# Kernel tuning notes

Hardware: AMD Instinct MI355X
Metric: run time of the kernel (lower is better)

The kernel has to match this reference:

```python
import jax, jax.numpy as jnp
import numpy as np

V, D, T, B, MS, WIN, EOS = 10000, 256, 128, 8, 4, 1, 4
S = MS + 1          # decoder segment length (y_input0 + MAX_SEGMENT tokens)
HRATE = 0.1
LOGINF = 1e6


def setup_inputs() -> dict:
    key = jax.random.key(0)
    ks = jax.random.split(key, 17)
    s = lambda i, shape: (jax.random.normal(ks[i], shape, jnp.float32) * 0.05)
    return dict(
        x_ids=jax.random.randint(ks[0], (B, T + 2 * WIN), 0, V),
        lens=jnp.full((B,), T, dtype=jnp.int32),
        emb=s(1, (V, D)),
        y_start=s(2, (1, D)),
        cell_Wi=s(3, (4 * D, D)), cell_Wh=s(4, (4 * D, D)), cell_b=s(5, (4 * D,)),
        yin0_W=s(6, (D, D)), yin0_b=s(7, (D,)),
        hlin_W=s(8, (2 * D, D)), hlin_b=s(9, (2 * D,)),
        l0_Wi=s(10, (4 * D, D)), l0_Wh=s(11, (4 * D, D)), l0_b=s(12, (4 * D,)),
        l1_Wi=s(13, (4 * D, D)), l1_Wh=s(14, (4 * D, D)), l1_b=s(15, (4 * D,)),
        out_b=s(16, (V,)),
    )


def _cell(x, h, c, Wi, Wh, b):
    # torch LSTM gate order: i, f, g, o
    g = x @ Wi.T + h @ Wh.T + b
    i, f, gg, o = jnp.split(g, 4, axis=-1)
    c2 = jax.nn.sigmoid(f) * c + jax.nn.sigmoid(i) * jnp.tanh(gg)
    return jax.nn.sigmoid(o) * jnp.tanh(c2), c2


def reference(x_ids, lens, emb, y_start, cell_Wi, cell_Wh, cell_b,
              yin0_W, yin0_b, hlin_W, hlin_b,
              l0_Wi, l0_Wh, l0_b, l1_Wi, l1_Wh, l1_b, out_b):
    y = x_ids[:, WIN:-WIN]                     # [B, T] target ids
    x = emb[y]                                 # [B, T, D]

    # --- encoder LSTMCell scan over j_start (state persists across schedule) ---
    seq = jnp.concatenate(
        [jnp.broadcast_to(y_start, (B, D))[None], jnp.transpose(x, (1, 0, 2))[:-1]], 0)  # [T,B,D]
    z = jnp.zeros((B, D), x.dtype)
    def enc_step(carry, xt):
        h, c = carry
        h2, c2 = _cell(xt, h, c, cell_Wi, cell_Wh, cell_b)
        return (h2, c2), h2
    _, h_seq = jax.lax.scan(enc_step, (z, z), seq)        # [T, B, D]

    drop_h = HRATE * h_seq
    y_in0 = drop_h @ yin0_W.T + yin0_b                    # [T, B, D]
    h0_all = jnp.tanh(drop_h @ hlin_W.T + hlin_b).reshape(T, B, 2, D)  # per-layer init h

    # --- build decoder inputs [T, B, S, D]: (y_input0, x[j_start:j_start+MS]) ---
    xp = jnp.pad(x, ((0, 0), (0, MS), (0, 0)))            # zero-pad time (causal => pads don't affect valid outputs)
    pos = jnp.arange(T)[:, None] + jnp.arange(MS)[None, :]           # [T, MS]
    seg_x = jnp.transpose(xp[:, pos], (1, 0, 2, 3))       # [T, B, MS, D]
    seg = jnp.concatenate([y_in0[:, :, None, :], seg_x], axis=2)     # [T, B, S, D]

    # --- 2-layer LSTM decoder, vmapped over j_start ---
    def decode(seg_t, h_init):                            # seg_t [B,S,D], h_init [B,2,D]
        def step(carry, xt):
            (h0, c0), (h1, c1) = carry
            h0n, c0n = _cell(xt, h0, c0, l0_Wi, l0_Wh, l0_b)
            h1n, c1n = _cell(h0n, h1, c1, l1_Wi, l1_Wh, l1_b)
            return ((h0n, c0n), (h1n, c1n)), h1n
        init = ((h_init[:, 0], z), (h_init[:, 1], z))
        _, hs = jax.lax.scan(step, init, jnp.transpose(seg_t, (1, 0, 2)))
        return jnp.transpose(hs, (1, 0, 2))               # [B, S, D]
    dec_h = jax.vmap(decode)(seg, h0_all)                 # [T, B, S, D]

    # --- tied output projection + log-softmax (only needed gathers kept) ---
    logits = jnp.einsum('tbsd,vd->tbsv', dec_h, emb) + out_b         # [T,B,S,V]
    logZ = jax.nn.logsumexp(logits, axis=-1)                          # [T,B,S]

    tgt = jnp.transpose(y[:, jnp.clip(pos, 0, T - 1)], (1, 0, 2))     # [T,B,MS]
    tgt_lp = jnp.take_along_axis(logits[:, :, :MS, :], tgt[..., None], axis=3)[..., 0] \
             - logZ[:, :, :MS]                                        # [T,B,MS]
    pmask = (pos < T)[:, None, :]
    cum = jnp.cumsum(jnp.where(pmask, tgt_lp, 0.0), axis=2)           # [T,B,MS]
    eos_lp = logits[:, :, 1:, EOS] - logZ[:, :, 1:]                   # [T,B,MS]

    kmask = (jnp.arange(T)[:, None] + jnp.arange(1, MS + 1)[None, :]) <= T   # [T,MS]
    body = jnp.where(kmask[:, None, :], cum + eos_lp, -LOGINF)        # [T,B,MS]
    logpy = jnp.concatenate([jnp.full((T, 1, B), -LOGINF, body.dtype),
                             jnp.transpose(body, (0, 2, 1))], axis=1)  # [T, MS+1, B]

    # --- alpha forward DP: alpha[j] = logsumexp_L alpha[j-L] + logpy[j-L][L] ---
    jj = jnp.arange(1, T + 1)[:, None]
    ii = jnp.arange(MS)[None, :]
    sstart = jj - MS + ii                                             # [T,MS]
    LPG = jnp.where((sstart >= 0)[..., None],
                    logpy[jnp.clip(sstart, 0), jnp.broadcast_to(MS - ii, (T, MS))],
                    -LOGINF)                                          # [T,MS,B]

    Apad0 = jnp.full((MS + T + 1, B), -LOGINF, logpy.dtype).at[MS].set(0.0)
    def dp_step(Apad, args):
        j, lpg = args
        win = jax.lax.dynamic_slice(Apad, (j, 0), (MS, B))            # alpha[j-MS .. j-1]
        aj = jax.nn.logsumexp(win + lpg, axis=0)
        return jax.lax.dynamic_update_slice(Apad, aj[None], (MS + j, 0)), None
    Apad, _ = jax.lax.scan(dp_step, Apad0, (jnp.arange(1, T + 1), LPG))
    alpha = Apad[MS:]                                                 # [T+1, B]

    ret = -jnp.sum(alpha[lens, jnp.arange(B)]) / jnp.sum(lens).astype(alpha.dtype)
    return ret
```

## Files before the change

kernel.cpp:

```cpp
#include <hip/hip_runtime.h>

#define V_ 10000
#define D_ 256
#define T_ 128
#define B_ 8
#define MS_ 4
#define S_ 5
#define EOS_ 4

typedef unsigned short b16_t;
typedef __attribute__((ext_vector_type(8))) short s16x8;
typedef __attribute__((ext_vector_type(8))) unsigned short u16x8;
typedef __attribute__((ext_vector_type(4))) float f32x4;
typedef __attribute__((ext_vector_type(2))) _Float16 h16x2;

__device__ inline b16_t f2bf(float f) {
  union { float f; unsigned u; } v; v.f = f;
  unsigned r = v.u + 0x7FFFu + ((v.u >> 16) & 1u);
  return (b16_t)(r >> 16);
}
__device__ inline float bf2f(b16_t h) {
  union { unsigned u; float f; } v; v.u = ((unsigned)h) << 16; return v.f;
}
__device__ inline float sigm_(float x) { return 1.0f / (1.0f + __expf(-x)); }
__device__ inline float tanh_(float x) { return 2.0f / (1.0f + __expf(-2.0f * x)) - 1.0f; }
__device__ inline h16x2 bch(unsigned u) { return __builtin_bit_cast(h16x2, u); }
__device__ inline unsigned pkh(float a, float b) {
  h16x2 v; v.x = (_Float16)a; v.y = (_Float16)b;
  return __builtin_bit_cast(unsigned, v);
}

#if __has_builtin(__builtin_amdgcn_fdot2)
#define FDOT2(a, b, c) __builtin_amdgcn_fdot2((a), (b), (c), false)
#else
#define FDOT2(a, b, c) ((c) + (float)(a).x * (float)(b).x + (float)(a).y * (float)(b).y)
#endif

__device__ inline float qswap1(float x) {
  return __builtin_bit_cast(float, __builtin_amdgcn_update_dpp(
      0, __builtin_bit_cast(int, x), 0xB1, 0xF, 0xF, true));
}

__device__ inline void cvt4(const float* __restrict__ s, b16_t* __restrict__ d) {
  float4 v = *(const float4*)s;
  ushort4 o = { f2bf(v.x), f2bf(v.y), f2bf(v.z), f2bf(v.w) };
  *(ushort4*)d = o;
}

__global__ void k_prep(const float* __restrict__ emb, const float* __restrict__ cWi,
                       const float* __restrict__ y0W, const float* __restrict__ hlW,
                       const float* __restrict__ l0Wi, const float* __restrict__ l0Wh,
                       const float* __restrict__ l1Wi, const float* __restrict__ l1Wh,
                       const float* __restrict__ cWh, const int* __restrict__ x_ids,
                       const float* __restrict__ y_st,
                       b16_t* __restrict__ emb_bf, b16_t* __restrict__ cWi_bf,
                       b16_t* __restrict__ y0W_bf, b16_t* __restrict__ hlW_bf,
                       b16_t* __restrict__ l0Wi_bf, b16_t* __restrict__ l0Wh_bf,
                       b16_t* __restrict__ Wcat_bf, unsigned* __restrict__ Whf,
                       b16_t* __restrict__ seq_bf, b16_t* __restrict__ seg_bf) {
  for (long i = (long)blockIdx.x * blockDim.x + threadIdx.x; i < 1410048L;
       i += (long)gridDim.x * blockDim.x) {
    if (i < 640000L) { cvt4(emb + i * 4, emb_bf + i * 4); }
    else if (i < 705536L) { long j = i - 640000L; cvt4(cWi + j * 4, cWi_bf + j * 4); }
    else if (i < 721920L) { long j = i - 705536L; cvt4(y0W + j * 4, y0W_bf + j * 4); }
    else if (i < 754688L) { long j = i - 721920L; cvt4(hlW + j * 4, hlW_bf + j * 4); }
    else if (i < 820224L) { long j = i - 754688L; cvt4(l0Wi + j * 4, l0Wi_bf + j * 4); }
    else if (i < 885760L) { long j = i - 820224L; cvt4(l0Wh + j * 4, l0Wh_bf + j * 4); }
    else if (i < 1016832L) {
      long j = (i - 885760L) * 4;
      long n = j >> 9; int k = (int)(j & 511);
      const float* src = (k < 256) ? (l1Wi + n * 256 + k) : (l1Wh + n * 256 + (k - 256));
      cvt4(src, Wcat_bf + j);
    } else if (i < 1082368L) {
      long j = i - 1016832L;
      float4 v = *(const float4*)(cWh + j * 4);
      Whf[2 * j] = pkh(v.x, v.y);
      Whf[2 * j + 1] = pkh(v.z, v.w);
    } else if (i < 1147904L) {
      long j = i - 1082368L;
      int m = (int)(j >> 6), c = (int)(j & 63) * 4;
      int t = m >> 3, b = m & 7;
      const float* src = (t == 0) ? (y_st + c)
                                  : (emb + (size_t)x_ids[b * (T_ + 2) + t] * D_ + c);
      cvt4(src, seq_bf + (size_t)m * D_ + c);
    } else {
      long j = i - 1147904L;
      int r = (int)(j >> 6), c = (int)(j & 63) * 4;
      int p = r >> 2, s = 1 + (r & 3);
      int t = p >> 3, b = p & 7;
      int tt = t + s - 1;
      int ps = r + (r >> 2) + 1;
      if (tt < T_) {
        int tok = x_ids[b * (T_ + 2) + tt + 1];
        cvt4(emb + (size_t)tok * D_ + c, seg_bf + (size_t)ps * 256 + c);
      } else {
        ushort4 z = {0, 0, 0, 0};
        *(ushort4*)(seg_bf + (size_t)ps * 256 + c) = z;
      }
    }
  }
}

__global__ __launch_bounds__(256) void k_gemm(const b16_t* __restrict__ A, int lda,
                                              const b16_t* __restrict__ Bw,
                                              const float* __restrict__ bias,
                                              float* __restrict__ C, int ldc) {
  __shared__ b16_t As[64][264];
  __shared__ b16_t Bs[64][264];
  int tid = threadIdx.x;
  int rowBase = blockIdx.x * 64, colBase = blockIdx.y * 64;
  for (int i = tid; i < 64 * 32; i += 256) {
    int r = i >> 5, c = (i & 31) * 8;
    *(u16x8*)&As[r][c] = *(const u16x8*)(A + (size_t)(rowBase + r) * lda + c);
    *(u16x8*)&Bs[r][c] = *(const u16x8*)(Bw + (size_t)(colBase + r) * 256 + c);
  }
  __syncthreads();
  int w = tid >> 6, l = tid & 63, lr = l & 15, kg = l >> 4;
  f32x4 acc[4] = {{0.f,0.f,0.f,0.f},{0.f,0.f,0.f,0.f},{0.f,0.f,0.f,0.f},{0.f,0.f,0.f,0.f}};
  for (int kk = 0; kk < 8; ++kk) {
    s16x8 a = *(const s16x8*)&As[w * 16 + lr][kk * 32 + kg * 8];
#pragma unroll
    for (int f = 0; f < 4; ++f) {
      s16x8 b = *(const s16x8*)&Bs[f * 16 + lr][kk * 32 + kg * 8];
      acc[f] = __builtin_amdgcn_mfma_f32_16x16x32_bf16(a, b, acc[f], 0, 0, 0);
    }
  }
#pragma unroll
  for (int f = 0; f < 4; ++f) {
#pragma unroll
    for (int r = 0; r < 4; ++r) {
      int m = rowBase + w * 16 + kg * 4 + r;
      int n = colBase + f * 16 + lr;
      C[(size_t)m * ldc + n] = acc[f][r] + bias[n];
    }
  }
}

#define ENC_CH4(i0)                                                            \
  do {                                                                         \
    uint4 a0 = hp[i0], a1 = hp[i0 + 1], a2 = hp[i0 + 2], a3 = hp[i0 + 3];      \
    s0 = FDOT2(bch(a0.x), bch(wv[4 * (i0) + 0]), s0);                          \
    s1 = FDOT2(bch(a0.y), bch(wv[4 * (i0) + 1]), s1);                          \
    s0 = FDOT2(bch(a0.z), bch(wv[4 * (i0) + 2]), s0);                          \
    s1 = FDOT2(bch(a0.w), bch(wv[4 * (i0) + 3]), s1);                          \
    s0 = FDOT2(bch(a1.x), bch(wv[4 * (i0) + 4]), s0);                          \
    s1 = FDOT2(bch(a1.y), bch(wv[4 * (i0) + 5]), s1);                          \
    s0 = FDOT2(bch(a1.z), bch(wv[4 * (i0) + 6]), s0);                          \
    s1 = FDOT2(bch(a1.w), bch(wv[4 * (i0) + 7]), s1);                          \
    s0 = FDOT2(bch(a2.x), bch(wv[4 * (i0) + 8]), s0);                          \
    s1 = FDOT2(bch(a2.y), bch(wv[4 * (i0) + 9]), s1);                          \
    s0 = FDOT2(bch(a2.z), bch(wv[4 * (i0) + 10]), s0);                         \
    s1 = FDOT2(bch(a2.w), bch(wv[4 * (i0) + 11]), s1);                         \
    s0 = FDOT2(bch(a3.x), bch(wv[4 * (i0) + 12]), s0);                         \
    s1 = FDOT2(bch(a3.y), bch(wv[4 * (i0) + 13]), s1);                         \
    s0 = FDOT2(bch(a3.z), bch(wv[4 * (i0) + 14]), s0);                         \
    s1 = FDOT2(bch(a3.w), bch(wv[4 * (i0) + 15]), s1);                         \
  } while (0)

struct EncS { unsigned hbuf[128]; float gl[256]; };
struct GemS { b16_t As[64][264]; b16_t Bs[64][264]; };

__global__ __launch_bounds__(512, 2) void k_enc_x0(
    const unsigned* __restrict__ Whf,
    const float* __restrict__ encX,
    unsigned* __restrict__ hglob,
    b16_t* __restrict__ droph,
    const b16_t* __restrict__ seg_bf, const b16_t* __restrict__ l0Wi_bf,
    const float* __restrict__ l0b, float* __restrict__ X0) {
  __shared__ union { EncS e; GemS g; } sm;
  int tid = threadIdx.x;
  if (blockIdx.x < 32) {
    int b = blockIdx.x & 7, q = blockIdx.x >> 3;
    int r = tid >> 1, ch = tid & 1;
    int growr = ((r >> 6) << 8) + q * 64 + (r & 63);
    unsigned wv[64];
    {
      const uint4* wp = (const uint4*)(Whf + (size_t)growr * 128 + ch * 64);
#pragma unroll
      for (int i = 0; i < 16; ++i) {
        uint4 v = wp[i];
        wv[4*i] = v.x; wv[4*i+1] = v.y; wv[4*i+2] = v.z; wv[4*i+3] = v.w;
      }
    }
#pragma unroll
    for (int i = 0; i < 64; ++i) asm volatile("" : "+v"(wv[i]));
    if (tid < 128) sm.e.hbuf[tid] = 0;
    float c = 0.f;
    float ex = encX[(size_t)b * 1024 + growr];
    __syncthreads();
#pragma unroll 1
    for (int t = 0; t < 128; ++t) {
      const uint4* hp = (const uint4*)&sm.e.hbuf[ch * 64];
      float s0 = 0.f, s1 = 0.f;
      ENC_CH4(0);
      __builtin_amdgcn_sched_barrier(0);
      ENC_CH4(4);
      __builtin_amdgcn_sched_barrier(0);
      ENC_CH4(8);
      __builtin_amdgcn_sched_barrier(0);
      ENC_CH4(12);
      float sum = s0 + s1;
      sum += qswap1(sum);
      if (ch == 0) sm.e.gl[r] = sum + ex;
      __syncthreads();
      if (tid < 64) {
        float gi = sm.e.gl[tid], gf = sm.e.gl[64 + tid];
        float gg = sm.e.gl[128 + tid], go = sm.e.gl[192 + tid];
        float c2 = sigm_(gf) * c + sigm_(gi) * tanh_(gg);
        float h2 = sigm_(go) * tanh_(c2);
        c = c2;
        float hnb = qswap1(h2);
        if ((tid & 1) == 0) {
          unsigned pk = pkh(h2, hnb) | 0x00010001u;
          sm.e.hbuf[q * 32 + (tid >> 1)] = pk;
          if (t < 127)
            __hip_atomic_store(&hglob[(((size_t)t * 8 + b) * 4 + q) * 32 + (tid >> 1)],
                               pk, __ATOMIC_RELAXED, __HIP_MEMORY_SCOPE_AGENT);
        }
        droph[((size_t)t * 8 + b) * 256 + q * 64 + tid] = f2bf(0.1f * h2);
      }
      if (t < 127) {
        if (tid >= 64 && tid < 160) {
          int idx = tid - 64;
          int ro = idx >> 5;
          int rq = ro + (ro >= q);
          int dw = idx & 31;
          unsigned* src = &hglob[(((size_t)t * 8 + b) * 4 + rq) * 32 + dw];
          unsigned v;
          do {
            v = __hip_atomic_load(src, __ATOMIC_RELAXED, __HIP_MEMORY_SCOPE_AGENT);
          } while (v == 0u);
          sm.e.hbuf[rq * 32 + dw] = v;
        }
        ex = encX[((size_t)(t + 1) * 8 + b) * 1024 + growr];
        __syncthreads();
      }
    }
  } else {
    int bx2 = blockIdx.x - 32;
    int rb = (bx2 & 63) * 64;
    int colBase = (bx2 >> 6) * 64;
    if (tid < 256) {
      for (int i = tid; i < 64 * 32; i += 256) {
        int r = i >> 5, cc = (i & 31) * 8;
        int jj = rb + r, ps = jj + (jj >> 2) + 1;
        *(u16x8*)&sm.g.As[r][cc] = *(const u16x8*)(seg_bf + (size_t)ps * 256 + cc);
        *(u16x8*)&sm.g.Bs[r][cc] = *(const u16x8*)(l0Wi_bf + (size_t)(colBase + r) * 256 + cc);
      }
    }
    __syncthreads();
    if (tid < 256) {
      int w = tid >> 6, l = tid & 63, lr = l & 15, kg = l >> 4;
      f32x4 acc[4] = {{0.f,0.f,0.f,0.f},{0.f,0.f,0.f,0.f},{0.f,0.f,0.f,0.f},{0.f,0.f,0.f,0.f}};
      for (int kk = 0; kk < 8; ++kk) {
        s16x8 a = *(const s16x8*)&sm.g.As[w * 16 + lr][kk * 32 + kg * 8];
#pragma unroll
        for (int f = 0; f < 4; ++f) {
          s16x8 b = *(const s16x8*)&sm.g.Bs[f * 16 + lr][kk * 32 + kg * 8];
          acc[f] = __builtin_amdgcn_mfma_f32_16x16x32_bf16(a, b, acc[f], 0, 0, 0);
        }
      }
#pragma unroll
      for (int f = 0; f < 4; ++f) {
#pragma unroll
        for (int r = 0; r < 4; ++r) {
          int jj = rb + w * 16 + kg * 4 + r;
          int ps = jj + (jj >> 2) + 1;
          int n = colBase + f * 16 + lr;
          X0[(size_t)ps * 1024 + n] = acc[f][r] + l0b[n];
        }
      }
    }
  }
}

__global__ __launch_bounds__(256) void k_proj(
    const b16_t* __restrict__ droph, const b16_t* __restrict__ y0W_bf,
    const float* __restrict__ y0b, const b16_t* __restrict__ hlW_bf,
    const float* __restrict__ hlb, b16_t* __restrict__ seg_bf,
    b16_t* __restrict__ hcat,
    const b16_t* __restrict__ l0Wi_bf, const float* __restrict__ l0b,
    float* __restrict__ X0) {
  __shared__ b16_t As[64][264];
  __shared__ b16_t Bs[64][264];
  int bx = blockIdx.x, by = blockIdx.y;
  const b16_t* Ab; int lda;
  const b16_t* Bw; const float* bias; int colBase, mode;
  if (by < 4)       { Ab = droph;  lda = 256;  Bw = y0W_bf;  bias = y0b; colBase = by * 64;        mode = 0; }
  else if (by < 12) { Ab = droph;  lda = 256;  Bw = hlW_bf;  bias = hlb; colBase = (by - 4) * 64;  mode = 1; }
  else              { Ab = seg_bf; lda = 1280; Bw = l0Wi_bf; bias = l0b; colBase = (by - 12) * 64; mode = 2; }
  int rowBase = bx * 64;
  int tid = threadIdx.x;
  for (int i = tid; i < 64 * 32; i += 256) {
    int r = i >> 5, c = (i & 31) * 8;
    *(u16x8*)&As[r][c] = *(const u16x8*)(Ab + (size_t)(rowBase + r) * lda + c);
    *(u16x8*)&Bs[r][c] = *(const u16x8*)(Bw + (size_t)(colBase + r) * 256 + c);
  }
  __syncthreads();
  int w = tid >> 6, l = tid & 63, lr = l & 15, kg = l >> 4;
  f32x4 acc[4] = {{0.f,0.f,0.f,0.f},{0.f,0.f,0.f,0.f},{0.f,0.f,0.f,0.f},{0.f,0.f,0.f,0.f}};
  for (int kk = 0; kk < 8; ++kk) {
    s16x8 a = *(const s16x8*)&As[w * 16 + lr][kk * 32 + kg * 8];
#pragma unroll
    for (int f = 0; f < 4; ++f) {
      s16x8 b = *(const s16x8*)&Bs[f * 16 + lr][kk * 32 + kg * 8];
      acc[f] = __builtin_amdgcn_mfma_f32_16x16x32_bf16(a, b, acc[f], 0, 0, 0);
    }
  }
#pragma unroll
  for (int f = 0; f < 4; ++f) {
#pragma unroll
    for (int r = 0; r < 4; ++r) {
      int m = rowBase + w * 16 + kg * 4 + r;
      int n = colBase + f * 16 + lr;
      float v = acc[f][r] + bias[n];
      if (mode == 0) seg_bf[(size_t)m * 1280 + n] = f2bf(v);
      else if (mode == 1) hcat[(size_t)m * 512 + n] = f2bf(tanh_(v));
      else X0[(size_t)m * 5120 + n] = v;
    }
  }
}

__global__ __launch_bounds__(512) void k_dec2(
    b16_t* __restrict__ hcat,
    const b16_t* __restrict__ l0Wh_bf,
    const b16_t* __restrict__ Wcat_bf,
    const float* __restrict__ X0,
    const float* __restrict__ l1b,
    float* __restrict__ c0, float* __restrict__ c1,
    b16_t* __restrict__ dec_out, int s) {
  __shared__ b16_t A0s[16][264];
  __shared__ b16_t A1s[16][520];
  int tid = threadIdx.x;
  int R0 = blockIdx.x * 16;
  for (int i = tid; i < 16 * 32; i += 512) {
    int r = i >> 5, cc = (i & 31) * 8;
    *(u16x8*)&A0s[r][cc] = *(const u16x8*)(hcat + (size_t)(R0 + r) * 512 + cc);
    *(u16x8*)&A1s[r][256 + cc] = *(const u16x8*)(hcat + (size_t)(R0 + r) * 512 + 256 + cc);
  }
  __syncthreads();
  int w = tid >> 6, l = tid & 63, lr = l & 15, kg = l >> 4;
  {
    s16x8 af[8];
#pragma unroll
    for (int kk = 0; kk < 8; ++kk)
      af[kk] = *(const s16x8*)&A0s[lr][kk * 32 + kg * 8];
    f32x4 acc[4][2];
#pragma unroll
    for (int g = 0; g < 4; ++g)
#pragma unroll
      for (int ct = 0; ct < 2; ++ct) acc[g][ct] = f32x4{0.f, 0.f, 0.f, 0.f};
#pragma unroll
    for (int g = 0; g < 4; ++g)
#pragma unroll
      for (int ct = 0; ct < 2; ++ct) {
        int n = g * 256 + w * 32 + ct * 16 + lr;
        const b16_t* bp = l0Wh_bf + (size_t)n * 256 + kg * 8;
#pragma unroll
        for (int kk = 0; kk < 8; ++kk)
          acc[g][ct] = __builtin_amdgcn_mfma_f32_16x16x32_bf16(
              af[kk], *(const s16x8*)(bp + kk * 32), acc[g][ct], 0, 0, 0);
      }
#pragma unroll
    for (int ct = 0; ct < 2; ++ct)
#pragma unroll
      for (int r = 0; r < 4; ++r) {
        int row = kg * 4 + r, p = R0 + row, d = w * 32 + ct * 16 + lr;
        const float* xp = X0 + ((size_t)p * 5 + s) * 1024;
        float gi = acc[0][ct][r] + xp[d],       gf = acc[1][ct][r] + xp[256 + d];
        float gg = acc[2][ct][r] + xp[512 + d], go = acc[3][ct][r] + xp[768 + d];
        float cc0 = c0[(size_t)p * 256 + d];
        float c2 = sigm_(gf) * cc0 + sigm_(gi) * tanh_(gg);
        float h2 = sigm_(go) * tanh_(c2);
        c0[(size_t)p * 256 + d] = c2;
        b16_t hb = f2bf(h2);
        A1s[row][d] = hb;
        hcat[(size_t)p * 512 + d] = hb;
      }
  }
  __syncthreads();
  {
    s16x8 a1[16];
#pragma unroll
    for (int kk = 0; kk < 16; ++kk)
      a1[kk] = *(const s16x8*)&A1s[lr][kk * 32 + kg * 8];
    f32x4 acc[4][2];
#pragma unroll
    for (int g = 0; g < 4; ++g)
#pragma unroll
      for (int ct = 0; ct < 2; ++ct) acc[g][ct] = f32x4{0.f, 0.f, 0.f, 0.f};
#pragma unroll
    for (int g = 0; g < 4; ++g)
#pragma unroll
      for (int ct = 0; ct < 2; ++ct) {
        int n = g * 256 + w * 32 + ct * 16 + lr;
        const b16_t* bp = Wcat_bf + (size_t)n * 512 + kg * 8;
#pragma unroll
        for (int kk = 0; kk < 16; ++kk)
          acc[g][ct] = __builtin_amdgcn_mfma_f32_16x16x32_bf16(
              a1[kk], *(const s16x8*)(bp + kk * 32), acc[g][ct], 0, 0, 0);
      }
#pragma unroll
    for (int ct = 0; ct < 2; ++ct)
#pragma unroll
      for (int r = 0; r < 4; ++r) {
        int row = kg * 4 + r, p = R0 + row, d = w * 32 + ct * 16 + lr;
        float gi = acc[0][ct][r] + l1b[d],       gf = acc[1][ct][r] + l1b[256 + d];
        float gg = acc[2][ct][r] + l1b[512 + d], go = acc[3][ct][r] + l1b[768 + d];
        float cc1 = c1[(size_t)p * 256 + d];
        float c2 = sigm_(gf) * cc1 + sigm_(gi) * tanh_(gg);
        float h2 = sigm_(go) * tanh_(c2);
        c1[(size_t)p * 256 + d] = c2;
        b16_t hb = f2bf(h2);
        hcat[(size_t)p * 512 + 256 + d] = hb;
        dec_out[((size_t)p * 5 + s) * 256 + d] = hb;
      }
  }
}

__global__ __launch_bounds__(512) void k_logits_ext(
    const b16_t* __restrict__ Abf, const b16_t* __restrict__ emb_bf,
    const float* __restrict__ out_b, float* __restrict__ sumexp,
    const int* __restrict__ x_ids, float* __restrict__ tl,
    float* __restrict__ el) {
  int bid = blockIdx.x;
  int tid = threadIdx.x;
  if (bid < 560) {
    __shared__ b16_t Bs[64][264];
    int rowBase = (bid % 40) * 128;
    int w = tid >> 6, l = tid & 63, lr = l & 15, kg = l >> 4;
    s16x8 af[8];
    {
      const b16_t* arow = Abf + (size_t)(rowBase + w * 16 + lr) * 256;
#pragma unroll
      for (int kk = 0; kk < 8; ++kk) af[kk] = *(const s16x8*)(arow + kk * 32 + kg * 8);
    }
    float runsum[4] = {0.f, 0.f, 0.f, 0.f};
    int t0 = (bid / 40) * 12, t1 = (t0 + 12 < 157) ? (t0 + 12) : 157;
    for (int tile = t0; tile < t1; ++tile) {
      int colBase = tile * 64;
      __syncthreads();
      for (int i = tid; i < 64 * 32; i += 512) {
        int r = i >> 5, cc = (i & 31) * 8;
        int vrow = colBase + r;
        u16x8 bv = {0, 0, 0, 0, 0, 0, 0, 0};
        if (vrow < V_) bv = *(const u16x8*)(emb_bf + (size_t)vrow * D_ + cc);
        *(u16x8*)&Bs[r][cc] = bv;
      }
      __syncthreads();
      f32x4 acc[4] = {{0.f,0.f,0.f,0.f},{0.f,0.f,0.f,0.f},{0.f,0.f,0.f,0.f},{0.f,0.f,0.f,0.f}};
#pragma unroll
      for (int kk = 0; kk < 8; ++kk) {
#pragma unroll
        for (int f = 0; f < 4; ++f) {
          s16x8 b = *(const s16x8*)&Bs[f * 16 + lr][kk * 32 + kg * 8];
          acc[f] = __builtin_amdgcn_mfma_f32_16x16x32_bf16(af[kk], b, acc[f], 0, 0, 0);
        }
      }
#pragma unroll
      for (int f = 0; f < 4; ++f) {
        int n = colBase + f * 16 + lr;
        if (n < V_) {
          float ob = out_b[n];
#pragma unroll
          for (int r = 0; r < 4; ++r) runsum[r] += __expf(acc[f][r] + ob);
        }
      }
    }
#pragma unroll
    for (int r = 0; r < 4; ++r) {
      float rs = runsum[r];
      rs += __shfl_xor(rs, 1, 64);
      rs += __shfl_xor(rs, 2, 64);
      rs += __shfl_xor(rs, 4, 64);
      rs += __shfl_xor(rs, 8, 64);
      if (lr == 0) atomicAdd(&sumexp[rowBase + w * 16 + kg * 4 + r], rs);
    }
  } else {
    int p = (bid - 560) * 8 + (tid >> 6);
    int lane = tid & 63;
    int t = p >> 3, b = p & 7;
    for (int s = 0; s < S_; ++s) {
      const b16_t* hr = Abf + ((size_t)p * S_ + s) * D_;
      float hv[4];
#pragma unroll
      for (int j = 0; j < 4; ++j) hv[j] = bf2f(hr[lane * 4 + j]);
      if (s < MS_) {
        int pos = t + s; if (pos > T_ - 1) pos = T_ - 1;
        int tok = x_ids[b * (T_ + 2) + pos + 1];
        const b16_t* er = emb_bf + (size_t)tok * D_;
        float ps = 0.f;
#pragma unroll
        for (int j = 0; j < 4; ++j) ps += hv[j] * bf2f(er[lane * 4 + j]);
        for (int m = 1; m < 64; m <<= 1) ps += __shfl_xor(ps, m, 64);
        if (lane == 0) tl[p * MS_ + s] = ps + out_b[tok];
      }
      if (s >= 1) {
        const b16_t* er = emb_bf + (size_t)EOS_ * D_;
        float ps = 0.f;
#pragma unroll
        for (int j = 0; j < 4; ++j) ps += hv[j] * bf2f(er[lane * 4 + j]);
        for (int m = 1; m < 64; m <<= 1) ps += __shfl_xor(ps, m, 64);
        if (lane == 0) el[p * MS_ + (s - 1)] = ps + out_b[EOS_];
      }
    }
  }
}

__global__ __launch_bounds__(256) void k_final(const float* __restrict__ sumexp,
                                               const float* __restrict__ tl,
                                               const float* __restrict__ el,
                                               const int* __restrict__ lens,
                                               float* __restrict__ out) {
  __shared__ float logpy[T_][S_][B_];
  __shared__ float alpha[T_ + 1][B_];
  int tid = threadIdx.x;
  for (int p = tid; p < T_ * B_; p += 256) {
    int t = p >> 3, b = p & 7;
    float lz[S_];
#pragma unroll
    for (int s = 0; s < S_; ++s) lz[s] = __logf(sumexp[p * S_ + s]);
    float cum = 0.f, cums[MS_];
#pragma unroll
    for (int s = 0; s < MS_; ++s) {
      float tlp = tl[p * MS_ + s] - lz[s];
      if (t + s < T_) cum += tlp;
      cums[s] = cum;
    }
#pragma unroll
    for (int k = 1; k <= MS_; ++k) {
      float bv = -1000000.0f;
      if (t + k <= T_) bv = cums[k - 1] + (el[p * MS_ + (k - 1)] - lz[k]);
      logpy[t][k][b] = bv;
    }
  }
  __syncthreads();
  if (tid < B_) {
    int b = tid;
    alpha[0][b] = 0.f;
    for (int j = 1; j <= T_; ++j) {
      float vs[MS_], vmax = -1e30f;
#pragma unroll
      for (int k = 1; k <= MS_; ++k) {
        float vv = -2000000.0f;
        if (j - k >= 0) vv = alpha[j - k][b] + logpy[j - k][k][b];
        vs[k - 1] = vv;
        if (vv > vmax) vmax = vv;
      }
      float ssum = 0.f;
#pragma unroll
      for (int k = 0; k < MS_; ++k) ssum += __expf(vs[k] - vmax);
      alpha[j][b] = vmax + __logf(ssum);
    }
  }
  __syncthreads();
  if (tid == 0) {
    float num = 0.f, den = 0.f;
    for (int b = 0; b < B_; ++b) { num += alpha[lens[b]][b]; den += (float)lens[b]; }
    out[0] = -num / den;
  }
}

extern "C" void kernel_launch(void* const* d_in, const int* in_sizes, int n_in,
                              void* d_out, int out_size, void* d_ws, size_t ws_size,
                              hipStream_t stream) {
  const int* x_ids   = (const int*)d_in[0];
  const int* lens    = (const int*)d_in[1];
  const float* emb   = (const float*)d_in[2];
  const float* y_st  = (const float*)d_in[3];
  const float* cWi   = (const float*)d_in[4];
  const float* cWh   = (const float*)d_in[5];
  const float* cb    = (const float*)d_in[6];
  const float* y0W   = (const float*)d_in[7];
  const float* y0b   = (const float*)d_in[8];
  const float* hlW   = (const float*)d_in[9];
  const float* hlb   = (const float*)d_in[10];
  const float* l0Wi  = (const float*)d_in[11];
  const float* l0Wh  = (const float*)d_in[12];
  const float* l0b   = (const float*)d_in[13];
  const float* l1Wi  = (const float*)d_in[14];
  const float* l1Wh  = (const float*)d_in[15];
  const float* l1b   = (const float*)d_in[16];
  const float* outb  = (const float*)d_in[17];
  float* out = (float*)d_out;
  (void)in_sizes; (void)n_in; (void)out_size; (void)ws_size;

  char* ws = (char*)d_ws;
  size_t cur = 0;
  auto alloc = [&](size_t bytes) { size_t o = cur; cur += (bytes + 255) & ~(size_t)255; return o; };
  b16_t* emb_bf    = (b16_t*)(ws + alloc((size_t)V_ * D_ * 2));
  b16_t* cWi_bf    = (b16_t*)(ws + alloc(1024 * 256 * 2));
  b16_t* y0W_bf    = (b16_t*)(ws + alloc(256 * 256 * 2));
  b16_t* hlW_bf    = (b16_t*)(ws + alloc(512 * 256 * 2));
  b16_t* l0Wi_bf   = (b16_t*)(ws + alloc(1024 * 256 * 2));
  b16_t* l0Wh_bf   = (b16_t*)(ws + alloc(1024 * 256 * 2));
  b16_t* Wcat_bf   = (b16_t*)(ws + alloc(1024 * 512 * 2));
  unsigned* Whf    = (unsigned*)(ws + alloc(1024 * 128 * 4));
  b16_t* seq_bf    = (b16_t*)(ws + alloc(1024 * 256 * 2));
  float* encX      = (float*)(ws + alloc((size_t)1024 * 1024 * 4));
  b16_t* droph_bf  = (b16_t*)(ws + alloc(1024 * 256 * 2));
  b16_t* hcat      = (b16_t*)(ws + alloc(1024 * 512 * 2));
  b16_t* seg_bf    = (b16_t*)(ws + alloc((size_t)5120 * 256 * 2));
  float* X0        = (float*)(ws + alloc((size_t)5120 * 1024 * 4));
  float* c0        = (float*)(ws + alloc((size_t)2 * 1024 * 256 * 4));
  float* c1        = c0 + 1024 * 256;
  b16_t* dec_h_bf  = (b16_t*)(ws + alloc((size_t)5120 * 256 * 2));
  float* sumexp    = (float*)(ws + alloc(5120 * 4));
  unsigned* hglob  = (unsigned*)(ws + alloc((size_t)128 * 8 * 4 * 32 * 4));
  float* tl        = (float*)(ws + alloc(1024 * MS_ * 4));
  float* el        = (float*)(ws + alloc(1024 * MS_ * 4));

  hipMemsetAsync(sumexp, 0, 20480 + 524288, stream);
  hipMemsetAsync(c0, 0, (size_t)2 * 1024 * 256 * 4, stream);

  k_prep<<<1024, 256, 0, stream>>>(emb, cWi, y0W, hlW, l0Wi, l0Wh, l1Wi, l1Wh, cWh,
                                   x_ids, y_st,
                                   emb_bf, cWi_bf, y0W_bf, hlW_bf, l0Wi_bf, l0Wh_bf,
                                   Wcat_bf, Whf, seq_bf, seg_bf);

  k_gemm<<<dim3(16, 16), 256, 0, stream>>>(seq_bf, 256, cWi_bf, cb, encX, 1024);
  k_enc_x0<<<1056, 512, 0, stream>>>(Whf, encX, hglob, droph_bf,
                                     seg_bf, l0Wi_bf, l0b, X0);

  k_proj<<<dim3(16, 28), 256, 0, stream>>>(droph_bf, y0W_bf, y0b, hlW_bf, hlb,
                                           seg_bf, hcat, l0Wi_bf, l0b, X0);

  for (int s = 0; s < S_; ++s)
    k_dec2<<<64, 512, 0, stream>>>(hcat, l0Wh_bf, Wcat_bf, X0, l1b, c0, c1, dec_h_bf, s);

  k_logits_ext<<<688, 512, 0, stream>>>(dec_h_bf, emb_bf, outb, sumexp,
                                        x_ids, tl, el);
  k_final<<<1, 256, 0, stream>>>(sumexp, tl, el, lens, out);
}
```

Measured before the change: 556.6 us.

## Split encoder recurrent matvec into 2 rows x quarter-K per thread

Each encoder thread now computes partial dot products for two adjacent gate rows over one quarter of the hidden vector, instead of one row over half of it. Every h value read from LDS then feeds two rows, which halves the LDS traffic and shortens the dependent load chain in the 128-step serial recurrence. The partial sums are reduced across four lanes with two DPP swaps. The hbuf array is padded to a stride of 36 words per chunk so the four quarter readers avoid LDS bank conflicts. The cost is an extra reduction step and slightly more complex indexing.

Result: no change. 546.6 us (-1.8%).

```diff
diff --git a/kernel.cpp b/kernel.cpp
--- a/kernel.cpp
+++ b/kernel.cpp
@@ -39,6 +39,10 @@
 __device__ inline float qswap1(float x) {
   return __builtin_bit_cast(float, __builtin_amdgcn_update_dpp(
       0, __builtin_bit_cast(int, x), 0xB1, 0xF, 0xF, true));
+}
+__device__ inline float qswap2(float x) {
+  return __builtin_bit_cast(float, __builtin_amdgcn_update_dpp(
+      0, __builtin_bit_cast(int, x), 0x4E, 0xF, 0xF, true));
 }
 
 __device__ inline void cvt4(const float* __restrict__ s, b16_t* __restrict__ d) {
@@ -136,28 +140,44 @@
   }
 }
 
-#define ENC_CH4(i0)                                                            \
+#define ENC_Q4(i0)                                                             \
   do {                                                                         \
     uint4 a0 = hp[i0], a1 = hp[i0 + 1], a2 = hp[i0 + 2], a3 = hp[i0 + 3];      \
     s0 = FDOT2(bch(a0.x), bch(wv[4 * (i0) + 0]), s0);                          \
-    s1 = FDOT2(bch(a0.y), bch(wv[4 * (i0) + 1]), s1);                          \
+    s1 = FDOT2(bch(a0.x), bch(wv[32 + 4 * (i0) + 0]), s1);                     \
+    s0 = FDOT2(bch(a0.y), bch(wv[4 * (i0) + 1]), s0);                          \
+    s1 = FDOT2(bch(a0.y), bch(wv[32 + 4 * (i0) + 1]), s1);                     \
     s0 = FDOT2(bch(a0.z), bch(wv[4 * (i0) + 2]), s0);                          \
-    s1 = FDOT2(bch(a0.w), bch(wv[4 * (i0) + 3]), s1);                          \
+    s1 = FDOT2(bch(a0.z), bch(wv[32 + 4 * (i0) + 2]), s1);                     \
+    s0 = FDOT2(bch(a0.w), bch(wv[4 * (i0) + 3]), s0);                          \
+    s1 = FDOT2(bch(a0.w), bch(wv[32 + 4 * (i0) + 3]), s1);                     \
     s0 = FDOT2(bch(a1.x), bch(wv[4 * (i0) + 4]), s0);                          \
-    s1 = FDOT2(bch(a1.y), bch(wv[4 * (i0) + 5]), s1);                          \
+    s1 = FDOT2(bch(a1.x), bch(wv[32 + 4 * (i0) + 4]), s1);                     \
+    s0 = FDOT2(bch(a1.y), bch(wv[4 * (i0) + 5]), s0);                          \
+    s1 = FDOT2(bch(a1.y), bch(wv[32 + 4 * (i0) + 5]), s1);                     \
     s0 = FDOT2(bch(a1.z), bch(wv[4 * (i0) + 6]), s0);                          \
-    s1 = FDOT2(bch(a1.w), bch(wv[4 * (i0) + 7]), s1);                          \
+    s1 = FDOT2(bch(a1.z), bch(wv[32 + 4 * (i0) + 6]), s1);                     \
+    s0 = FDOT2(bch(a1.w), bch(wv[4 * (i0) + 7]), s0);                          \
+    s1 = FDOT2(bch(a1.w), bch(wv[32 + 4 * (i0) + 7]), s1);                     \
     s0 = FDOT2(bch(a2.x), bch(wv[4 * (i0) + 8]), s0);                          \
-    s1 = FDOT2(bch(a2.y), bch(wv[4 * (i0) + 9]), s1);                          \
+    s1 = FDOT2(bch(a2.x), bch(wv[32 + 4 * (i0) + 8]), s1);                     \
+    s0 = FDOT2(bch(a2.y), bch(wv[4 * (i0) + 9]), s0);                          \
+    s1 = FDOT2(bch(a2.y), bch(wv[32 + 4 * (i0) + 9]), s1);                     \
     s0 = FDOT2(bch(a2.z), bch(wv[4 * (i0) + 10]), s0);                         \
-    s1 = FDOT2(bch(a2.w), bch(wv[4 * (i0) + 11]), s1);                         \
+    s1 = FDOT2(bch(a2.z), bch(wv[32 + 4 * (i0) + 10]), s1);                    \
+    s0 = FDOT2(bch(a2.w), bch(wv[4 * (i0) + 11]), s0);                         \
+    s1 = FDOT2(bch(a2.w), bch(wv[32 + 4 * (i0) + 11]), s1);                    \
     s0 = FDOT2(bch(a3.x), bch(wv[4 * (i0) + 12]), s0);                         \
-    s1 = FDOT2(bch(a3.y), bch(wv[4 * (i0) + 13]), s1);                         \
+    s1 = FDOT2(bch(a3.x), bch(wv[32 + 4 * (i0) + 12]), s1);                    \
+    s0 = FDOT2(bch(a3.y), bch(wv[4 * (i0) + 13]), s0);                         \
+    s1 = FDOT2(bch(a3.y), bch(wv[32 + 4 * (i0) + 13]), s1);                    \
     s0 = FDOT2(bch(a3.z), bch(wv[4 * (i0) + 14]), s0);                         \
-    s1 = FDOT2(bch(a3.w), bch(wv[4 * (i0) + 15]), s1);                         \
+    s1 = FDOT2(bch(a3.z), bch(wv[32 + 4 * (i0) + 14]), s1);                    \
+    s0 = FDOT2(bch(a3.w), bch(wv[4 * (i0) + 15]), s0);                         \
+    s1 = FDOT2(bch(a3.w), bch(wv[32 + 4 * (i0) + 15]), s1);                    \
   } while (0)
 
-struct EncS { unsigned hbuf[128]; float gl[256]; };
+struct EncS { unsigned hbuf[144]; float gl[256]; };
 struct GemS { b16_t As[64][264]; b16_t Bs[64][264]; };
 
 __global__ __launch_bounds__(512, 2) void k_enc_x0(
@@ -171,37 +191,41 @@
   int tid = threadIdx.x;
   if (blockIdx.x < 32) {
     int b = blockIdx.x & 7, q = blockIdx.x >> 3;
-    int r = tid >> 1, ch = tid & 1;
-    int growr = ((r >> 6) << 8) + q * 64 + (r & 63);
+    int rp = tid >> 2, cq = tid & 3;
+    int r0l = 2 * rp;
+    int grow0 = ((r0l >> 6) << 8) + q * 64 + (r0l & 63);
     unsigned wv[64];
     {
-      const uint4* wp = (const uint4*)(Whf + (size_t)growr * 128 + ch * 64);
-#pragma unroll
-      for (int i = 0; i < 16; ++i) {
-        uint4 v = wp[i];
+      const uint4* wp0 = (const uint4*)(Whf + (size_t)grow0 * 128 + cq * 32);
+      const uint4* wp1 = (const uint4*)(Whf + (size_t)(grow0 + 1) * 128 + cq * 32);
+#pragma unroll
+      for (int i = 0; i < 8; ++i) {
+        uint4 v = wp0[i];
         wv[4*i] = v.x; wv[4*i+1] = v.y; wv[4*i+2] = v.z; wv[4*i+3] = v.w;
       }
+#pragma unroll
+      for (int i = 0; i < 8; ++i) {
+        uint4 v = wp1[i];
+        wv[32+4*i] = v.x; wv[32+4*i+1] = v.y; wv[32+4*i+2] = v.z; wv[32+4*i+3] = v.w;
+      }
     }
 #pragma unroll
     for (int i = 0; i < 64; ++i) asm volatile("" : "+v"(wv[i]));
-    if (tid < 128) sm.e.hbuf[tid] = 0;
+    if (tid < 144) sm.e.hbuf[tid] = 0;
     float c = 0.f;
-    float ex = encX[(size_t)b * 1024 + growr];
+    float ex = encX[(size_t)b * 1024 + grow0 + (cq & 1)];
     __syncthreads();
 #pragma unroll 1
     for (int t = 0; t < 128; ++t) {
-      const uint4* hp = (const uint4*)&sm.e.hbuf[ch * 64];
+      const uint4* hp = (const uint4*)&sm.e.hbuf[cq * 36];
       float s0 = 0.f, s1 = 0.f;
-      ENC_CH4(0);
+      ENC_Q4(0);
       __builtin_amdgcn_sched_barrier(0);
-      ENC_CH4(4);
-      __builtin_amdgcn_sched_barrier(0);
-      ENC_CH4(8);
-      __builtin_amdgcn_sched_barrier(0);
-      ENC_CH4(12);
-      float sum = s0 + s1;
-      sum += qswap1(sum);
-      if (ch == 0) sm.e.gl[r] = sum + ex;
+      ENC_Q4(4);
+      s0 += qswap1(s0); s0 += qswap2(s0);
+      s1 += qswap1(s1); s1 += qswap2(s1);
+      if (cq == 0) sm.e.gl[r0l] = s0 + ex;
+      else if (cq == 1) sm.e.gl[r0l + 1] = s1 + ex;
       __syncthreads();
       if (tid < 64) {
         float gi = sm.e.gl[tid], gf = sm.e.gl[64 + tid];
@@ -212,7 +236,7 @@
         float hnb = qswap1(h2);
         if ((tid & 1) == 0) {
           unsigned pk = pkh(h2, hnb) | 0x00010001u;
-          sm.e.hbuf[q * 32 + (tid >> 1)] = pk;
+          sm.e.hbuf[q * 36 + (tid >> 1)] = pk;
           if (t < 127)
             __hip_atomic_store(&hglob[(((size_t)t * 8 + b) * 4 + q) * 32 + (tid >> 1)],
                                pk, __ATOMIC_RELAXED, __HIP_MEMORY_SCOPE_AGENT);
@@ -230,9 +254,9 @@
           do {
             v = __hip_atomic_load(src, __ATOMIC_RELAXED, __HIP_MEMORY_SCOPE_AGENT);
           } while (v == 0u);
-          sm.e.hbuf[rq * 32 + dw] = v;
+          sm.e.hbuf[rq * 36 + dw] = v;
         }
-        ex = encX[((size_t)(t + 1) * 8 + b) * 1024 + growr];
+        ex = encX[((size_t)(t + 1) * 8 + b) * 1024 + grow0 + (cq & 1)];
         __syncthreads();
       }
     }
```
